# Kernel optimization log

Hardware: AMD Instinct MI355X
Metric: run time of the kernel (lower is better)

The kernel has to match this reference:

```python
import jax, jax.numpy as jnp
import numpy as np

N, T, E, E2 = 10000, 32, 320000, 160000
D, H = 128, 128
SLOPE = 0.01  # LeakyReLU negative slope (args.relu)


def _lstm_dir(x, mask, Wih, Whh, b, reverse):
    # x: [N,T,D], mask: [N,T] int; returns final hidden [N,H] honoring per-seq lengths
    xs = jnp.swapaxes(x, 0, 1)                                 # [T,N,D]
    ms = jnp.swapaxes(mask, 0, 1)[..., None].astype(x.dtype)   # [T,N,1]
    Hh = Whh.shape[1]
    h0 = jnp.zeros((x.shape[0], Hh), x.dtype)

    def step(carry, tm):
        h, c = carry
        xt, mt = tm
        g = xt @ Wih.T + h @ Whh.T + b                         # [N,4H], torch gate order i,f,g,o
        i, f, gg, o = jnp.split(g, 4, axis=-1)
        i, f, o = jax.nn.sigmoid(i), jax.nn.sigmoid(f), jax.nn.sigmoid(o)
        c_new = f * c + i * jnp.tanh(gg)
        h_new = o * jnp.tanh(c_new)
        h = mt * h_new + (1.0 - mt) * h
        c = mt * c_new + (1.0 - mt) * c
        return (h, c), None

    (h, _), _ = jax.lax.scan(step, (h0, h0), (xs, ms), reverse=reverse)
    return h


def _sage(h, src, dst, Wself, Wneigh, b):
    # DGL SAGEConv, mean aggregator: h@W_self + mean_neigh(h)@W_neigh + b
    n = h.shape[0]
    msum = jax.ops.segment_sum(h[src], dst, num_segments=n)
    deg = jax.ops.segment_sum(jnp.ones((src.shape[0],), h.dtype), dst, num_segments=n)
    neigh = msum / jnp.maximum(deg, 1.0)[:, None]
    return h @ Wself + neigh @ Wneigh + b


def setup_inputs():
    key = jax.random.key(0)
    ks = jax.random.split(key, 40)
    f = lambda i, shape: jax.random.normal(ks[i], shape, jnp.float32) * 0.05
    return dict(
        inputs_s=jax.random.randint(ks[0], (N, T), 0, 128, jnp.int32),
        inputs_sm=jnp.ones((N, T), jnp.int32),
        inputs_c=jax.random.randint(ks[1], (N,), 0, 101, jnp.int32),
        inputs_co=jax.random.randint(ks[2], (N,), 0, 92, jnp.int32),
        inputs_sl=jax.random.randint(ks[3], (N,), 0, 6, jnp.int32),
        inputs_ip=jax.random.normal(ks[4], (N, 32), jnp.float32),
        blk_src=jax.random.randint(ks[5], (E,), 0, N, jnp.int32),
        blk_dst=jax.random.randint(ks[6], (E,), 0, N, jnp.int32),
        e_src=jax.random.randint(ks[7], (E2,), 0, N, jnp.int32),
        e_dst=jax.random.randint(ks[8], (E2,), 0, N, jnp.int32),
        emb_url=f(9, (128, D)), emb_cat=f(10, (101, D)), emb_cou=f(11, (92, D)), emb_sl_t=f(12, (6, D)),
        Wih_f=f(13, (4 * D, D)), Whh_f=f(14, (4 * D, D)), b_f=f(15, (4 * D,)),
        Wih_b=f(16, (4 * D, D)), Whh_b=f(17, (4 * D, D)), b_b=f(18, (4 * D,)),
        fc_lstm_W=f(19, (2 * D, D)), fc_lstm_b=f(20, (D,)),
        attnlin_W=f(21, (H, H)), attn_W=f(22, (H, 1)), attn_b=f(23, (1,)),
        W0_self=f(24, (4, D, H)), W0_neigh=f(25, (4, D, H)), b0=f(26, (4, H)),
        Wip_self=f(27, (32, H)), Wip_neigh=f(28, (32, H)), bip=f(29, (H,)),
        W1_self=f(30, (5, H, H)), W1_neigh=f(31, (5, H, H)), b1=f(32, (5, H)),
        fc_W=f(33, (2 * H, H)), fc_b=f(34, (H,)),
        fco_W=f(35, (H, 2)), fco_b=f(36, (2,)),
    )


def reference(inputs_s, inputs_sm, inputs_c, inputs_co, inputs_sl, inputs_ip,
              blk_src, blk_dst, e_src, e_dst,
              emb_url, emb_cat, emb_cou, emb_sl_t,
              Wih_f, Whh_f, b_f, Wih_b, Whh_b, b_b,
              fc_lstm_W, fc_lstm_b, attnlin_W, attn_W, attn_b,
              W0_self, W0_neigh, b0, Wip_self, Wip_neigh, bip,
              W1_self, W1_neigh, b1, fc_W, fc_b, fco_W, fco_b):
    lrelu = lambda x: jax.nn.leaky_relu(x, SLOPE)
    # --- URL encoder: embed -> bi-LSTM -> fc (dropout is identity in eval) ---
    xu = emb_url[inputs_s]                                      # [N,T,D]
    hf = _lstm_dir(xu, inputs_sm, Wih_f, Whh_f, b_f, False)     # fwd final hidden
    hb = _lstm_dir(xu, inputs_sm, Wih_b, Whh_b, b_b, True)      # bwd final hidden
    vec_url = lrelu(jnp.concatenate([hf, hb], 1) @ fc_lstm_W + fc_lstm_b)
    # --- six-stream (here five: no rules) SAGE stacks over shared blocks ---
    h4 = jnp.stack([vec_url, emb_cat[inputs_c], emb_cou[inputs_co], emb_sl_t[inputs_sl]])  # [4,N,D]
    sage_v = jax.vmap(_sage, in_axes=(0, None, None, 0, 0, 0))
    h4 = lrelu(sage_v(h4, blk_src, blk_dst, W0_self, W0_neigh, b0))
    hip = lrelu(_sage(inputs_ip, blk_src, blk_dst, Wip_self, Wip_neigh, bip))
    hs = jnp.concatenate([h4, hip[None]], 0)                    # [5,N,H]
    hs = lrelu(sage_v(hs, blk_src, blk_dst, W1_self, W1_neigh, b1))
    hs = jnp.transpose(hs, (1, 0, 2))                           # [N,5,H]
    # --- attention fusion across streams ---
    z = jnp.einsum('nsh,ho->nso', hs, attnlin_W)                # attn_linear(h_stack)
    a = jax.nn.softmax(jnp.einsum('nso,om->nsm', z, attn_W) + attn_b, axis=1)  # [N,5,1]
    h = jnp.sum(z * a, axis=1)                                  # [N,H]
    # --- per-edge gather-concat-MLP scoring (apply_edges) ---
    cat = jnp.concatenate([h[e_src], h[e_dst]], 1)              # [E2,2H]
    score = lrelu(cat @ fc_W + fc_b) @ fco_W + fco_b            # [E2,2]
    a_src = a[e_src][..., 0]                                    # [E2,5]
    attn_e = jnp.stack([a_src, a_src], axis=1)                  # [E2,2,5]
    return score, attn_e
```

## Files before the change

### kernel.cpp

```cpp
#include <hip/hip_runtime.h>
#include <hip/hip_bf16.h>
#include <stdint.h>

typedef unsigned short u16;
typedef unsigned int   u32;
typedef __attribute__((ext_vector_type(8))) short short8;
typedef __attribute__((ext_vector_type(4))) float f32x4;
typedef __attribute__((ext_vector_type(2))) u32   u32x2;
typedef __attribute__((ext_vector_type(4))) u32   u32x4;

#define DEV static __device__ __forceinline__

constexpr int N_  = 10000;
constexpr int T_  = 32;
constexpr int E_  = 320000;
constexpr int E2_ = 160000;

DEV u16 f2bf(float f) {
    union { float f; u32 u; } v; v.f = f;
    u32 u = v.u;
    return (u16)((u + 0x7fffu + ((u >> 16) & 1u)) >> 16);
}
DEV float bf2f(u16 h) {
    union { u32 u; float f; } v; v.u = ((u32)h) << 16; return v.f;
}
DEV float asf(u32 u) {
    union { u32 u; float f; } v; v.u = u; return v.f;
}
DEV u32 cvt_pk_bf16(float lo, float hi) {
    u32 r;
    asm("v_cvt_pk_bf16_f32 %0, %1, %2" : "=v"(r) : "v"(lo), "v"(hi));
    return r;
}
DEV float lrelu(float x) { return x > 0.f ? x : 0.01f * x; }

DEV float fexp2(float x) {
#if __has_builtin(__builtin_amdgcn_exp2f)
    return __builtin_amdgcn_exp2f(x);
#else
    return exp2f(x);
#endif
}
DEV float frcp(float x) {
#if __has_builtin(__builtin_amdgcn_rcpf)
    return __builtin_amdgcn_rcpf(x);
#else
    return 1.0f / x;
#endif
}
DEV float fsig(float x)  { return frcp(1.f + fexp2(-1.4426950408889634f * x)); }
DEV float ftanh_(float x){ return 1.f - 2.f * frcp(1.f + fexp2(2.8853900817779268f * x)); }

__global__ void k_xtab(const float* __restrict__ emb,
                       const float* __restrict__ WihF, const float* __restrict__ bF,
                       const float* __restrict__ WihB, const float* __restrict__ bB,
                       u16* __restrict__ xtab) {
    int sym = blockIdx.x, dir = blockIdx.y, o = threadIdx.x;
    const float* W = dir ? WihB : WihF;
    const float* b = dir ? bB : bF;
    __shared__ float er[128];
    if (o < 128) er[o] = emb[sym * 128 + o];
    __syncthreads();
    float s = b[o];
    for (int k = 0; k < 128; k++) s += er[k] * W[o * 128 + k];
    xtab[((size_t)(dir * 128 + sym)) * 512 + o] = f2bf(s);
}

struct WtSeg { const float* W; u16* out; int Kd, Ks, Nw, tot; };
struct WtArgs { WtSeg seg[9]; };
__global__ void k_wt_all(WtArgs a) {
    WtSeg sg = a.seg[blockIdx.y];
    int i = blockIdx.x * 256 + threadIdx.x;
    if (i >= sg.tot) return;
    int k = i % sg.Kd, n = (i / sg.Kd) % sg.Nw, s = i / (sg.Kd * sg.Nw);
    float v = (k < sg.Ks) ? sg.W[((size_t)s * sg.Ks + k) * sg.Nw + n] : 0.f;
    sg.out[i] = f2bf(v);
}

__global__ __launch_bounds__(512, 2) void k_lstm(
    const u16* __restrict__ xtab,
    const int* __restrict__ syms,
    const int* __restrict__ smask,
    const float* __restrict__ WhhF,
    const float* __restrict__ WhhB,
    u16* __restrict__ hcat)
{
    __shared__ u16 h_buf0[2048];
    __shared__ u16 h_buf1[2048];
    __shared__ int sym_l[512];
    __shared__ int msk_l[512];

    int tid = threadIdx.x;
    int w = tid >> 6, l = tid & 63, l15 = l & 15, lg = l >> 4;
    int dir = blockIdx.y;
    int n0 = blockIdx.x * 16;
    const float* Whh = dir ? WhhB : WhhF;

    for (int i = tid; i < 512; i += 512) {
        int seq = i >> 5, t = i & 31;
        sym_l[t * 16 + seq] = syms[(size_t)n0 * 32 + i];
        msk_l[t * 16 + seq] = smask[(size_t)n0 * 32 + i];
    }
    for (int i = tid; i < 2048; i += 512) h_buf0[i] = 0;

    short8 aw[4][4];
#pragma unroll
    for (int gg = 0; gg < 4; gg++)
#pragma unroll
    for (int kk = 0; kk < 4; kk++) {
        const float* p = Whh + (size_t)(128 * gg + 16 * w + l15) * 128 + 32 * kk + 8 * lg;
        const float4* pp = (const float4*)p;
        float4 x0 = pp[0], x1 = pp[1];
        short8 v;
        v[0] = (short)f2bf(x0.x); v[1] = (short)f2bf(x0.y);
        v[2] = (short)f2bf(x0.z); v[3] = (short)f2bf(x0.w);
        v[4] = (short)f2bf(x1.x); v[5] = (short)f2bf(x1.y);
        v[6] = (short)f2bf(x1.z); v[7] = (short)f2bf(x1.w);
        aw[gg][kk] = v;
    }

    float hreg[4] = {0, 0, 0, 0};
    float creg[4] = {0, 0, 0, 0};
    int jb = 16 * w + 4 * lg;
    int wsk = 2 * w + (lg >> 1);
    int wof = (wsk * 16 + l15) * 8 + 4 * (lg & 1);
    const u16* xbase = xtab + (size_t)dir * 128 * 512 + jb;
    __syncthreads();

    u32x2 xt[4];
    {
        int t0 = dir ? 31 : 0;
        int sym0 = sym_l[t0 * 16 + l15];
        const u16* xr = xbase + (size_t)sym0 * 512;
#pragma unroll
        for (int gg = 0; gg < 4; gg++) xt[gg] = *(const u32x2*)(xr + gg * 128);
    }

    auto step = [&](int st, const u16* rb, u16* wb) {
        int t = dir ? (31 - st) : st;

        short8 bh[4];
#pragma unroll
        for (int kk = 0; kk < 4; kk++)
            bh[kk] = *(const short8*)&rb[((kk * 4 + lg) * 16 + l15) * 8];

        f32x4 acc[4];
#pragma unroll
        for (int gg = 0; gg < 4; gg++) {
            f32x4 a = { asf(xt[gg][0] << 16), asf(xt[gg][0] & 0xffff0000u),
                        asf(xt[gg][1] << 16), asf(xt[gg][1] & 0xffff0000u) };
#pragma unroll
            for (int kk = 0; kk < 4; kk++)
                a = __builtin_amdgcn_mfma_f32_16x16x32_bf16(aw[gg][kk], bh[kk], a, 0, 0, 0);
            acc[gg] = a;
        }

        {
            int stn = (st < 31) ? (st + 1) : 31;
            int tn = dir ? (31 - stn) : stn;
            int symn = sym_l[tn * 16 + l15];
            const u16* xr = xbase + (size_t)symn * 512;
#pragma unroll
            for (int gg = 0; gg < 4; gg++) xt[gg] = *(const u32x2*)(xr + gg * 128);
        }

        int mt_i = msk_l[t * 16 + l15];
        bool mb = mt_i != 0;
#pragma unroll
        for (int r = 0; r < 4; r++) {
            float i_ = fsig(acc[0][r]), f_ = fsig(acc[1][r]);
            float g_ = ftanh_(acc[2][r]), o_ = fsig(acc[3][r]);
            float cn = f_ * creg[r] + i_ * g_;
            float hn = o_ * ftanh_(cn);
            hreg[r] = mb ? hn : hreg[r];
            creg[r] = mb ? cn : creg[r];
        }
        u32x2 pk;
        pk[0] = cvt_pk_bf16(hreg[0], hreg[1]);
        pk[1] = cvt_pk_bf16(hreg[2], hreg[3]);
        *(u32x2*)&wb[wof] = pk;
        asm volatile("s_waitcnt lgkmcnt(0)" ::: "memory");
        __builtin_amdgcn_s_barrier();
    };

    for (int st2 = 0; st2 < 16; st2++) {
        step(2 * st2,     h_buf0, h_buf1);
        step(2 * st2 + 1, h_buf1, h_buf0);
    }

    {
        u32x2 pk;
        pk[0] = cvt_pk_bf16(hreg[0], hreg[1]);
        pk[1] = cvt_pk_bf16(hreg[2], hreg[3]);
        *(u32x2*)&hcat[(size_t)(n0 + l15) * 256 + dir * 128 + jb] = pk;
    }
}

template<int ACT, int DUAL>
__global__ __launch_bounds__(256) void k_gemm(
    const u16* __restrict__ A1, int lda1, int soA1,
    const u16* __restrict__ A2, int lda2, int soA2,
    const u16* __restrict__ B1, int soB1,
    const u16* __restrict__ B2, int soB2,
    const float* __restrict__ bias, int soBias,
    u16* __restrict__ C, int ldc, int soC, int M, int K)
{
    int s = blockIdx.y;
    A1 += (size_t)s * soA1;
    if (DUAL) A2 += (size_t)s * soA2;
    B1 += (size_t)s * soB1;
    if (DUAL) B2 += (size_t)s * soB2;
    if (bias) bias += (size_t)s * soBias;
    C += (size_t)s * soC;

    int tid = threadIdx.x;
    int w = tid >> 6, l = tid & 63, l15 = l & 15, lg = l >> 4;
    int mbase = blockIdx.x * 64 + w * 16;
    int arow = mbase + l15; if (arow >= M) arow = M - 1;

    f32x4 acc[8];
#pragma unroll
    for (int nt = 0; nt < 8; nt++) {
        float bv = bias ? bias[16 * nt + l15] : 0.f;
        acc[nt] = (f32x4){bv, bv, bv, bv};
    }
    for (int k0 = 0; k0 < K; k0 += 32) {
        int k = k0 + 8 * lg;
        short8 a1 = *(const short8*)&A1[(size_t)arow * lda1 + k];
        short8 a2;
        if (DUAL) a2 = *(const short8*)&A2[(size_t)arow * lda2 + k];
#pragma unroll
        for (int nt = 0; nt < 8; nt++) {
            short8 b1 = *(const short8*)&B1[(size_t)(16 * nt + l15) * K + k];
            acc[nt] = __builtin_amdgcn_mfma_f32_16x16x32_bf16(a1, b1, acc[nt], 0, 0, 0);
            if (DUAL) {
                short8 b2 = *(const short8*)&B2[(size_t)(16 * nt + l15) * K + k];
                acc[nt] = __builtin_amdgcn_mfma_f32_16x16x32_bf16(a2, b2, acc[nt], 0, 0, 0);
            }
        }
    }
#pragma unroll
    for (int nt = 0; nt < 8; nt++)
#pragma unroll
    for (int r = 0; r < 4; r++) {
        int m = mbase + 4 * lg + r;
        if (m < M) {
            float v = acc[nt][r];
            if (ACT == 1) v = lrelu(v);
            C[(size_t)m * ldc + 16 * nt + l15] = f2bf(v);
        }
    }
}

__global__ void k_pack(const int* __restrict__ ic, const int* __restrict__ ico,
                       const int* __restrict__ isl, const float* __restrict__ ip,
                       const float* __restrict__ ecat, const float* __restrict__ ecou,
                       const float* __restrict__ esl, u16* __restrict__ F0) {
    int n = blockIdx.x, t = threadIdx.x;
    u16* row = F0 + (size_t)n * 544;
    row[128 + t] = f2bf(ecat[(size_t)ic[n]  * 128 + t]);
    row[256 + t] = f2bf(ecou[(size_t)ico[n] * 128 + t]);
    row[384 + t] = f2bf(esl [(size_t)isl[n] * 128 + t]);
    if (t < 32) row[512 + t] = f2bf(ip[(size_t)n * 32 + t]);
}

__global__ void k_hist(const int* __restrict__ dst, int E, int* __restrict__ deg) {
    int e = blockIdx.x * 256 + threadIdx.x;
    if (e < E) atomicAdd(&deg[dst[e]], 1);
}
__global__ void k_scan(const int* __restrict__ deg, int* __restrict__ rowptr,
                       int* __restrict__ cursor, int n) {
    __shared__ int part[1024];
    int tid = threadIdx.x;
    const int CH = 10;
    int base = tid * CH;
    int s = 0;
#pragma unroll
    for (int i = 0; i < CH; i++) { int idx = base + i; if (idx < n) s += deg[idx]; }
    part[tid] = s; __syncthreads();
    for (int off = 1; off < 1024; off <<= 1) {
        int v = (tid >= off) ? part[tid - off] : 0;
        __syncthreads();
        part[tid] += v;
        __syncthreads();
    }
    int run = part[tid] - s;
    for (int i = 0; i < CH; i++) {
        int idx = base + i;
        if (idx < n) { rowptr[idx] = run; cursor[idx] = run; run += deg[idx]; }
    }
    if (tid == 1023) rowptr[n] = part[1023];
}
__global__ void k_fill(const int* __restrict__ src, const int* __restrict__ dst, int E,
                       int* __restrict__ cursor, int* __restrict__ colsrc) {
    int e = blockIdx.x * 256 + threadIdx.x;
    if (e < E) {
        int pos = atomicAdd(&cursor[dst[e]], 1);
        colsrc[pos] = src[e];
    }
}

__global__ __launch_bounds__(256) void k_agg(const u16* __restrict__ F, int C,
                                             const int* __restrict__ rowptr,
                                             const int* __restrict__ colsrc,
                                             u16* __restrict__ out, int N) {
    int w = threadIdx.x >> 6, l = threadIdx.x & 63;
    int n = blockIdx.x * 4 + w;
    if (n >= N) return;
    int chunks = C >> 3;
    int c0 = l, c1 = l + 64;
    bool has1 = c1 < chunks;
    float a0[8] = {0,0,0,0,0,0,0,0}, a1[8] = {0,0,0,0,0,0,0,0};
    int beg = rowptr[n], end = rowptr[n + 1];

    auto accum = [&](u32x4 v, float* a) {
#pragma unroll
        for (int j = 0; j < 4; j++) {
            u32 u = v[j];
            a[2*j]   += asf(u << 16);
            a[2*j+1] += asf(u & 0xffff0000u);
        }
    };

    int e = beg;
    for (; e + 8 <= end; e += 8) {
        const u32x4* rp[8];
#pragma unroll
        for (int j = 0; j < 8; j++)
            rp[j] = (const u32x4*)(F + (size_t)colsrc[e + j] * C);
        u32x4 v[8];
#pragma unroll
        for (int j = 0; j < 8; j++) v[j] = rp[j][c0];
        if (has1) {
            u32x4 u[8];
#pragma unroll
            for (int j = 0; j < 8; j++) u[j] = rp[j][c1];
#pragma unroll
            for (int j = 0; j < 8; j++) accum(v[j], a0);
#pragma unroll
            for (int j = 0; j < 8; j++) accum(u[j], a1);
        } else {
#pragma unroll
            for (int j = 0; j < 8; j++) accum(v[j], a0);
        }
    }
    for (; e + 4 <= end; e += 4) {
        const u32x4* rp[4];
#pragma unroll
        for (int j = 0; j < 4; j++)
            rp[j] = (const u32x4*)(F + (size_t)colsrc[e + j] * C);
        u32x4 v[4];
#pragma unroll
        for (int j = 0; j < 4; j++) v[j] = rp[j][c0];
        if (has1) {
            u32x4 u[4];
#pragma unroll
            for (int j = 0; j < 4; j++) u[j] = rp[j][c1];
#pragma unroll
            for (int j = 0; j < 4; j++) accum(v[j], a0);
#pragma unroll
            for (int j = 0; j < 4; j++) accum(u[j], a1);
        } else {
#pragma unroll
            for (int j = 0; j < 4; j++) accum(v[j], a0);
        }
    }
    for (; e < end; e++) {
        const u32x4* rp = (const u32x4*)(F + (size_t)colsrc[e] * C);
        accum(rp[c0], a0);
        if (has1) accum(rp[c1], a1);
    }

    int dg = end - beg; if (dg < 1) dg = 1;
    float inv = 1.f / (float)dg;
    u32x4 o0;
#pragma unroll
    for (int j = 0; j < 4; j++)
        o0[j] = (u32)f2bf(a0[2*j] * inv) | ((u32)f2bf(a0[2*j+1] * inv) << 16);
    ((u32x4*)(out + (size_t)n * C))[c0] = o0;
    if (has1) {
        u32x4 o1;
#pragma unroll
        for (int j = 0; j < 4; j++)
            o1[j] = (u32)f2bf(a1[2*j] * inv) | ((u32)f2bf(a1[2*j+1] * inv) << 16);
        ((u32x4*)(out + (size_t)n * C))[c1] = o1;
    }
}

__global__ __launch_bounds__(256) void k_attn(const u16* __restrict__ Z,
                                              const float* __restrict__ attnW,
                                              float* __restrict__ aOut,
                                              u16* __restrict__ hT, int N) {
    int w = threadIdx.x >> 6, l = threadIdx.x & 63;
    int n = blockIdx.x * 4 + w;
    if (n >= N) return;
    float wa0 = attnW[l], wa1 = attnW[l + 64];
    float z0[5], z1[5], lgt[5];
#pragma unroll
    for (int s = 0; s < 5; s++) {
        z0[s] = bf2f(Z[((size_t)(n * 5 + s)) * 128 + l]);
        z1[s] = bf2f(Z[((size_t)(n * 5 + s)) * 128 + l + 64]);
        float p = z0[s] * wa0 + z1[s] * wa1;
#pragma unroll
        for (int m = 1; m < 64; m <<= 1) p += __shfl_xor(p, m, 64);
        lgt[s] = p;
    }
    float mx = lgt[0];
#pragma unroll
    for (int s = 1; s < 5; s++) mx = fmaxf(mx, lgt[s]);
    float ex[5], sum = 0.f;
#pragma unroll
    for (int s = 0; s < 5; s++) { ex[s] = __expf(lgt[s] - mx); sum += ex[s]; }
    float a[5];
#pragma unroll
    for (int s = 0; s < 5; s++) a[s] = ex[s] / sum;
    float h0 = 0.f, h1 = 0.f;
#pragma unroll
    for (int s = 0; s < 5; s++) { h0 += a[s] * z0[s]; h1 += a[s] * z1[s]; }
    hT[(size_t)n * 128 + l] = f2bf(h0);
    hT[(size_t)n * 128 + l + 64] = f2bf(h1);
    if (l == 0) {
#pragma unroll
        for (int s = 0; s < 5; s++) aOut[(size_t)n * 5 + s] = a[s];
    }
}

__global__ __launch_bounds__(256) void k_edge(const u16* __restrict__ hT,
                                              const int* __restrict__ esrc,
                                              const int* __restrict__ edst,
                                              const u16* __restrict__ fcWt,
                                              const float* __restrict__ fcb,
                                              const float* __restrict__ fcoW,
                                              const float* __restrict__ fcob,
                                              const float* __restrict__ aA,
                                              float* __restrict__ score,
                                              float* __restrict__ attne,
                                              int E2) {
    int tid = threadIdx.x;
    int w = tid >> 6, l = tid & 63, l15 = l & 15, lg = l >> 4;
    int eb = (blockIdx.x * 4 + w) * 16;
    int arow = eb + l15; if (arow >= E2) arow = E2 - 1;
    int sn = esrc[arow], dn = edst[arow];

    f32x4 acc[8];
#pragma unroll
    for (int nt = 0; nt < 8; nt++) {
        float bv = fcb[16 * nt + l15];
        acc[nt] = (f32x4){bv, bv, bv, bv};
    }
#pragma unroll
    for (int kk = 0; kk < 8; kk++) {
        int k = 32 * kk + 8 * lg;
        const u16* ap = (k < 128) ? &hT[(size_t)sn * 128 + k]
                                  : &hT[(size_t)dn * 128 + (k - 128)];
        short8 a = *(const short8*)ap;
#pragma unroll
        for (int nt = 0; nt < 8; nt++) {
            short8 b = *(const short8*)&fcWt[(size_t)(16 * nt + l15) * 256 + k];
            acc[nt] = __builtin_amdgcn_mfma_f32_16x16x32_bf16(a, b, acc[nt], 0, 0, 0);
        }
    }
    float p0[4] = {0,0,0,0}, p1[4] = {0,0,0,0};
#pragma unroll
    for (int nt = 0; nt < 8; nt++) {
        int c = 16 * nt + l15;
        float w0 = fcoW[c * 2], w1 = fcoW[c * 2 + 1];
#pragma unroll
        for (int r = 0; r < 4; r++) {
            float hd = lrelu(acc[nt][r]);
            p0[r] += hd * w0; p1[r] += hd * w1;
        }
    }
#pragma unroll
    for (int m = 1; m < 16; m <<= 1) {
#pragma unroll
        for (int r = 0; r < 4; r++) {
            p0[r] += __shfl_xor(p0[r], m, 64);
            p1[r] += __shfl_xor(p1[r], m, 64);
        }
    }
    if (l15 == 0) {
        float b0v = fcob[0], b1v = fcob[1];
#pragma unroll
        for (int r = 0; r < 4; r++) {
            int e = eb + 4 * lg + r;
            if (e < E2) {
                score[(size_t)e * 2 + 0] = p0[r] + b0v;
                score[(size_t)e * 2 + 1] = p1[r] + b1v;
            }
        }
    }
#pragma unroll
    for (int pass = 0; pass < 3; pass++) {
        int idx = pass * 64 + l;
        if (idx < 160) {
            int e = eb + idx / 10;
            int j = idx % 10;
            int s = esrc[e];
            attne[(size_t)e * 10 + j] = aA[(size_t)s * 5 + (j >= 5 ? j - 5 : j)];
        }
    }
}

extern "C" void kernel_launch(void* const* d_in, const int* in_sizes, int n_in,
                              void* d_out, int out_size, void* d_ws, size_t ws_size,
                              hipStream_t stream) {
    const int* inp_s   = (const int*)d_in[0];
    const int* inp_sm  = (const int*)d_in[1];
    const int* inp_c   = (const int*)d_in[2];
    const int* inp_co  = (const int*)d_in[3];
    const int* inp_sl  = (const int*)d_in[4];
    const float* inp_ip = (const float*)d_in[5];
    const int* blk_src = (const int*)d_in[6];
    const int* blk_dst = (const int*)d_in[7];
    const int* e_src   = (const int*)d_in[8];
    const int* e_dst   = (const int*)d_in[9];
    const float* emb_url = (const float*)d_in[10];
    const float* emb_cat = (const float*)d_in[11];
    const float* emb_cou = (const float*)d_in[12];
    const float* emb_sl  = (const float*)d_in[13];
    const float* Wih_f = (const float*)d_in[14];
    const float* Whh_f = (const float*)d_in[15];
    const float* b_f   = (const float*)d_in[16];
    const float* Wih_b = (const float*)d_in[17];
    const float* Whh_b = (const float*)d_in[18];
    const float* b_b   = (const float*)d_in[19];
    const float* fc_lstm_W = (const float*)d_in[20];
    const float* fc_lstm_b = (const float*)d_in[21];
    const float* attnlin_W = (const float*)d_in[22];
    const float* attn_W    = (const float*)d_in[23];
    const float* W0_self  = (const float*)d_in[25];
    const float* W0_neigh = (const float*)d_in[26];
    const float* b0       = (const float*)d_in[27];
    const float* Wip_self  = (const float*)d_in[28];
    const float* Wip_neigh = (const float*)d_in[29];
    const float* bip       = (const float*)d_in[30];
    const float* W1_self  = (const float*)d_in[31];
    const float* W1_neigh = (const float*)d_in[32];
    const float* b1       = (const float*)d_in[33];
    const float* fc_W  = (const float*)d_in[34];
    const float* fc_b  = (const float*)d_in[35];
    const float* fco_W = (const float*)d_in[36];
    const float* fco_b = (const float*)d_in[37];

    char* ws = (char*)d_ws;
    size_t off = 0;
    auto alloc = [&](size_t bytes) -> char* {
        char* p = ws + off;
        off += (bytes + 255) & ~(size_t)255;
        return p;
    };
    u16* xtab      = (u16*)alloc((size_t)2 * 128 * 512 * 2);
    u16* hcat      = (u16*)alloc((size_t)N_ * 256 * 2);
    u16* wt_fclstm = (u16*)alloc((size_t)128 * 256 * 2);
    u16* wt_w05s   = (u16*)alloc((size_t)5 * 128 * 128 * 2);
    u16* wt_w05n   = (u16*)alloc((size_t)5 * 128 * 128 * 2);
    u16* wt_w1s    = (u16*)alloc((size_t)5 * 128 * 128 * 2);
    u16* wt_w1n    = (u16*)alloc((size_t)5 * 128 * 128 * 2);
    u16* wt_attn   = (u16*)alloc((size_t)128 * 128 * 2);
    u16* wt_fc     = (u16*)alloc((size_t)128 * 256 * 2);
    float* bias5   = (float*)alloc((size_t)5 * 128 * 4);
    u16* F0        = (u16*)alloc((size_t)N_ * 544 * 2);
    u16* NEI       = (u16*)alloc((size_t)N_ * 640 * 2);
    u16* F1        = (u16*)alloc((size_t)N_ * 640 * 2);
    u16* H1        = (u16*)alloc((size_t)N_ * 640 * 2);
    u16* Zb        = (u16*)alloc((size_t)N_ * 5 * 128 * 2);
    u16* hT        = (u16*)alloc((size_t)N_ * 128 * 2);
    float* aA      = (float*)alloc((size_t)N_ * 5 * 4);
    int* deg       = (int*)alloc((size_t)N_ * 4);
    int* rowptr    = (int*)alloc((size_t)(N_ + 1) * 4);
    int* cursor    = (int*)alloc((size_t)N_ * 4);
    int* colsrc    = (int*)alloc((size_t)E_ * 4);
    (void)ws_size; (void)in_sizes; (void)n_in; (void)out_size;

    float* out_score = (float*)d_out;
    float* out_attne = out_score + (size_t)2 * E2_;

    hipMemsetAsync(deg, 0, (size_t)N_ * 4, stream);
    k_hist<<<dim3((E_ + 255) / 256), dim3(256), 0, stream>>>(blk_dst, E_, deg);
    k_scan<<<dim3(1), dim3(1024), 0, stream>>>(deg, rowptr, cursor, N_);
    k_fill<<<dim3((E_ + 255) / 256), dim3(256), 0, stream>>>(blk_src, blk_dst, E_, cursor, colsrc);

    k_xtab<<<dim3(128, 2), dim3(512), 0, stream>>>(emb_url, Wih_f, b_f, Wih_b, b_b, xtab);
    {
        WtArgs a;
        a.seg[0] = {fc_lstm_W, wt_fclstm,            256, 256, 128, 1 * 128 * 256};
        a.seg[1] = {W0_self,   wt_w05s,              128, 128, 128, 4 * 128 * 128};
        a.seg[2] = {W0_neigh,  wt_w05n,              128, 128, 128, 4 * 128 * 128};
        a.seg[3] = {Wip_self,  wt_w05s + 4 * 16384,  128,  32, 128, 1 * 128 * 128};
        a.seg[4] = {Wip_neigh, wt_w05n + 4 * 16384,  128,  32, 128, 1 * 128 * 128};
        a.seg[5] = {W1_self,   wt_w1s,               128, 128, 128, 5 * 128 * 128};
        a.seg[6] = {W1_neigh,  wt_w1n,               128, 128, 128, 5 * 128 * 128};
        a.seg[7] = {attnlin_W, wt_attn,              128, 128, 128, 1 * 128 * 128};
        a.seg[8] = {fc_W,      wt_fc,                256, 256, 128, 1 * 128 * 256};
        k_wt_all<<<dim3((5 * 128 * 128 + 255) / 256, 9), dim3(256), 0, stream>>>(a);
    }
    hipMemcpyAsync(bias5, b0, 512 * sizeof(float), hipMemcpyDeviceToDevice, stream);
    hipMemcpyAsync(bias5 + 512, bip, 128 * sizeof(float), hipMemcpyDeviceToDevice, stream);

    k_lstm<<<dim3(N_ / 16, 2), dim3(512), 0, stream>>>(xtab, inp_s, inp_sm, Whh_f, Whh_b, hcat);

    k_gemm<1, 0><<<dim3((N_ + 63) / 64, 1), dim3(256), 0, stream>>>(
        hcat, 256, 0, nullptr, 0, 0, wt_fclstm, 0, nullptr, 0,
        fc_lstm_b, 0, F0, 544, 0, N_, 256);
    k_pack<<<dim3(N_), dim3(128), 0, stream>>>(inp_c, inp_co, inp_sl, inp_ip,
                                               emb_cat, emb_cou, emb_sl, F0);

    k_agg<<<dim3(N_ / 4), dim3(256), 0, stream>>>(F0, 544, rowptr, colsrc, NEI, N_);
    k_gemm<1, 1><<<dim3((N_ + 63) / 64, 5), dim3(256), 0, stream>>>(
        F0, 544, 128, NEI, 544, 128, wt_w05s, 128 * 128, wt_w05n, 128 * 128,
        bias5, 128, F1, 640, 128, N_, 128);

    k_agg<<<dim3(N_ / 4), dim3(256), 0, stream>>>(F1, 640, rowptr, colsrc, NEI, N_);
    k_gemm<1, 1><<<dim3((N_ + 63) / 64, 5), dim3(256), 0, stream>>>(
        F1, 640, 128, NEI, 640, 128, wt_w1s, 128 * 128, wt_w1n, 128 * 128,
        b1, 128, H1, 640, 128, N_, 128);

    k_gemm<0, 0><<<dim3((N_ * 5 + 63) / 64, 1), dim3(256), 0, stream>>>(
        H1, 128, 0, nullptr, 0, 0, wt_attn, 0, nullptr, 0,
        nullptr, 0, Zb, 128, 0, N_ * 5, 128);
    k_attn<<<dim3(N_ / 4), dim3(256), 0, stream>>>(Zb, attn_W, aA, hT, N_);

    k_edge<<<dim3(E2_ / 64), dim3(256), 0, stream>>>(hT, e_src, e_dst, wt_fc, fc_b,
                                                     fco_W, fco_b, aA,
                                                     out_score, out_attne, E2_);
}
```

Before: 587.4 us.

## Fuse attention GEMM with softmax, merge packing kernels, trim LSTM tail

Fuses the attention linear GEMM with the per-node softmax and weighted sum in one kernel that stages Z in shared memory, removing the Zb global round trip and one launch. Merges the fc_lstm GEMM and the embedding pack into one two-part launch, and folds the deg memset and bias copies into the weight-transpose kernel. Also skips the final LSTM step's h write and barrier and vectorizes the xtab weight loads. Each change removes launch overhead or memory traffic, at the cost of more complex kernels.

```diff
diff --git a/kernel.cpp b/kernel.cpp
--- a/kernel.cpp
+++ b/kernel.cpp
@@ -62,13 +62,28 @@
     if (o < 128) er[o] = emb[sym * 128 + o];
     __syncthreads();
     float s = b[o];
-    for (int k = 0; k < 128; k++) s += er[k] * W[o * 128 + k];
+    const float4* Wr = (const float4*)(W + (size_t)o * 128);
+    for (int k4 = 0; k4 < 32; k4++) {
+        float4 wv = Wr[k4];
+        s += er[4*k4]   * wv.x + er[4*k4+1] * wv.y
+           + er[4*k4+2] * wv.z + er[4*k4+3] * wv.w;
+    }
     xtab[((size_t)(dir * 128 + sym)) * 512 + o] = f2bf(s);
 }
 
 struct WtSeg { const float* W; u16* out; int Kd, Ks, Nw, tot; };
-struct WtArgs { WtSeg seg[9]; };
+struct WtArgs {
+    WtSeg seg[9];
+    int* deg; float* bias5; const float* b0; const float* bip;
+};
 __global__ void k_wt_all(WtArgs a) {
+    if (blockIdx.y == 9) {
+        int gid = blockIdx.x * 256 + threadIdx.x;
+        if (gid < N_) a.deg[gid] = 0;
+        int b = gid - 10240;
+        if (b >= 0 && b < 640) a.bias5[b] = (b < 512) ? a.b0[b] : a.bip[b - 512];
+        return;
+    }
     WtSeg sg = a.seg[blockIdx.y];
     int i = blockIdx.x * 256 + threadIdx.x;
     if (i >= sg.tot) return;
@@ -136,7 +151,7 @@
         for (int gg = 0; gg < 4; gg++) xt[gg] = *(const u32x2*)(xr + gg * 128);
     }
 
-    auto step = [&](int st, const u16* rb, u16* wb) {
+    auto step = [&](int st, const u16* rb, u16* wb, bool wr) {
         int t = dir ? (31 - st) : st;
 
         short8 bh[4];
@@ -155,8 +170,8 @@
             acc[gg] = a;
         }
 
-        {
-            int stn = (st < 31) ? (st + 1) : 31;
+        if (wr) {
+            int stn = st + 1;
             int tn = dir ? (31 - stn) : stn;
             int symn = sym_l[tn * 16 + l15];
             const u16* xr = xbase + (size_t)symn * 512;
@@ -175,18 +190,22 @@
             hreg[r] = mb ? hn : hreg[r];
             creg[r] = mb ? cn : creg[r];
         }
-        u32x2 pk;
-        pk[0] = cvt_pk_bf16(hreg[0], hreg[1]);
-        pk[1] = cvt_pk_bf16(hreg[2], hreg[3]);
-        *(u32x2*)&wb[wof] = pk;
-        asm volatile("s_waitcnt lgkmcnt(0)" ::: "memory");
-        __builtin_amdgcn_s_barrier();
+        if (wr) {
+            u32x2 pk;
+            pk[0] = cvt_pk_bf16(hreg[0], hreg[1]);
+            pk[1] = cvt_pk_bf16(hreg[2], hreg[3]);
+            *(u32x2*)&wb[wof] = pk;
+            asm volatile("s_waitcnt lgkmcnt(0)" ::: "memory");
+            __builtin_amdgcn_s_barrier();
+        }
     };
 
-    for (int st2 = 0; st2 < 16; st2++) {
-        step(2 * st2,     h_buf0, h_buf1);
-        step(2 * st2 + 1, h_buf1, h_buf0);
-    }
+    for (int st2 = 0; st2 < 15; st2++) {
+        step(2 * st2,     h_buf0, h_buf1, true);
+        step(2 * st2 + 1, h_buf1, h_buf0, true);
+    }
+    step(30, h_buf0, h_buf1, true);
+    step(31, h_buf1, h_buf0, false);
 
     {
         u32x2 pk;
@@ -252,16 +271,56 @@
     }
 }
 
-__global__ void k_pack(const int* __restrict__ ic, const int* __restrict__ ico,
-                       const int* __restrict__ isl, const float* __restrict__ ip,
-                       const float* __restrict__ ecat, const float* __restrict__ ecou,
-                       const float* __restrict__ esl, u16* __restrict__ F0) {
-    int n = blockIdx.x, t = threadIdx.x;
-    u16* row = F0 + (size_t)n * 544;
-    row[128 + t] = f2bf(ecat[(size_t)ic[n]  * 128 + t]);
-    row[256 + t] = f2bf(ecou[(size_t)ico[n] * 128 + t]);
-    row[384 + t] = f2bf(esl [(size_t)isl[n] * 128 + t]);
-    if (t < 32) row[512 + t] = f2bf(ip[(size_t)n * 32 + t]);
+__global__ __launch_bounds__(256) void k_fcpack(
+    const u16* __restrict__ hcat, const u16* __restrict__ Bt,
+    const float* __restrict__ bias, u16* __restrict__ F0,
+    const int* __restrict__ ic, const int* __restrict__ ico,
+    const int* __restrict__ isl, const float* __restrict__ ip,
+    const float* __restrict__ ecat, const float* __restrict__ ecou,
+    const float* __restrict__ esl, int M)
+{
+    if (blockIdx.y == 1) {
+        int gid = blockIdx.x * 256 + threadIdx.x;
+        const int TOT = N_ * 416;
+        for (int i = gid; i < TOT; i += 40192) {
+            int n = i / 416, c = i - n * 416;
+            float v;
+            if (c < 128)      v = ecat[(size_t)ic[n]  * 128 + c];
+            else if (c < 256) v = ecou[(size_t)ico[n] * 128 + (c - 128)];
+            else if (c < 384) v = esl [(size_t)isl[n] * 128 + (c - 256)];
+            else              v = ip  [(size_t)n * 32 + (c - 384)];
+            F0[(size_t)n * 544 + 128 + c] = f2bf(v);
+        }
+        return;
+    }
+    int tid = threadIdx.x;
+    int w = tid >> 6, l = tid & 63, l15 = l & 15, lg = l >> 4;
+    int mbase = blockIdx.x * 64 + w * 16;
+    int arow = mbase + l15; if (arow >= M) arow = M - 1;
+
+    f32x4 acc[8];
+#pragma unroll
+    for (int nt = 0; nt < 8; nt++) {
+        float bv = bias[16 * nt + l15];
+        acc[nt] = (f32x4){bv, bv, bv, bv};
+    }
+    for (int k0 = 0; k0 < 256; k0 += 32) {
+        int k = k0 + 8 * lg;
+        short8 a1 = *(const short8*)&hcat[(size_t)arow * 256 + k];
+#pragma unroll
+        for (int nt = 0; nt < 8; nt++) {
+            short8 b1 = *(const short8*)&Bt[(size_t)(16 * nt + l15) * 256 + k];
+            acc[nt] = __builtin_amdgcn_mfma_f32_16x16x32_bf16(a1, b1, acc[nt], 0, 0, 0);
+        }
+    }
+#pragma unroll
+    for (int nt = 0; nt < 8; nt++)
+#pragma unroll
+    for (int r = 0; r < 4; r++) {
+        int m = mbase + 4 * lg + r;
+        if (m < M)
+            F0[(size_t)m * 544 + 16 * nt + l15] = f2bf(lrelu(acc[nt][r]));
+    }
 }
 
 __global__ void k_hist(const int* __restrict__ dst, int E, int* __restrict__ deg) {
@@ -387,41 +446,84 @@
     }
 }
 
-__global__ __launch_bounds__(256) void k_attn(const u16* __restrict__ Z,
-                                              const float* __restrict__ attnW,
-                                              float* __restrict__ aOut,
-                                              u16* __restrict__ hT, int N) {
-    int w = threadIdx.x >> 6, l = threadIdx.x & 63;
-    int n = blockIdx.x * 4 + w;
-    if (n >= N) return;
-    float wa0 = attnW[l], wa1 = attnW[l + 64];
-    float z0[5], z1[5], lgt[5];
-#pragma unroll
-    for (int s = 0; s < 5; s++) {
-        z0[s] = bf2f(Z[((size_t)(n * 5 + s)) * 128 + l]);
-        z1[s] = bf2f(Z[((size_t)(n * 5 + s)) * 128 + l + 64]);
-        float p = z0[s] * wa0 + z1[s] * wa1;
-#pragma unroll
-        for (int m = 1; m < 64; m <<= 1) p += __shfl_xor(p, m, 64);
-        lgt[s] = p;
-    }
-    float mx = lgt[0];
-#pragma unroll
-    for (int s = 1; s < 5; s++) mx = fmaxf(mx, lgt[s]);
-    float ex[5], sum = 0.f;
-#pragma unroll
-    for (int s = 0; s < 5; s++) { ex[s] = __expf(lgt[s] - mx); sum += ex[s]; }
-    float a[5];
-#pragma unroll
-    for (int s = 0; s < 5; s++) a[s] = ex[s] / sum;
-    float h0 = 0.f, h1 = 0.f;
-#pragma unroll
-    for (int s = 0; s < 5; s++) { h0 += a[s] * z0[s]; h1 += a[s] * z1[s]; }
-    hT[(size_t)n * 128 + l] = f2bf(h0);
-    hT[(size_t)n * 128 + l + 64] = f2bf(h1);
-    if (l == 0) {
-#pragma unroll
-        for (int s = 0; s < 5; s++) aOut[(size_t)n * 5 + s] = a[s];
+__global__ __launch_bounds__(320) void k_zattn(
+    const u16* __restrict__ H1,
+    const u16* __restrict__ Bt,
+    const float* __restrict__ attnW,
+    float* __restrict__ aOut,
+    u16* __restrict__ hT)
+{
+    constexpr int ZP = 136;
+    __shared__ u16 zl[80 * ZP];
+    int tid = threadIdx.x;
+    int w = tid >> 6, l = tid & 63, l15 = l & 15, lg = l >> 4;
+    int rbase = blockIdx.x * 80 + w * 16;
+
+    f32x4 acc[8];
+#pragma unroll
+    for (int nt = 0; nt < 8; nt++) acc[nt] = (f32x4){0.f, 0.f, 0.f, 0.f};
+    for (int k0 = 0; k0 < 128; k0 += 32) {
+        int k = k0 + 8 * lg;
+        short8 a1 = *(const short8*)&H1[(size_t)(rbase + l15) * 128 + k];
+#pragma unroll
+        for (int nt = 0; nt < 8; nt++) {
+            short8 b1 = *(const short8*)&Bt[(size_t)(16 * nt + l15) * 128 + k];
+            acc[nt] = __builtin_amdgcn_mfma_f32_16x16x32_bf16(a1, b1, acc[nt], 0, 0, 0);
+        }
+    }
+#pragma unroll
+    for (int nt = 0; nt < 8; nt++)
+#pragma unroll
+    for (int r = 0; r < 4; r++)
+        zl[(w * 16 + 4 * lg + r) * ZP + 16 * nt + l15] = f2bf(acc[nt][r]);
+    __syncthreads();
+
+    if (tid < 256) {
+        int node = tid >> 4;
+        int j = tid & 15;
+        int d0 = j * 8;
+        float4 wa0 = *(const float4*)(attnW + d0);
+        float4 wa1 = *(const float4*)(attnW + d0 + 4);
+        float z[5][8], lgt[5];
+#pragma unroll
+        for (int s = 0; s < 5; s++) {
+            const u16* zr = &zl[(node * 5 + s) * ZP + d0];
+            u32x4 v = *(const u32x4*)zr;
+#pragma unroll
+            for (int q = 0; q < 4; q++) {
+                z[s][2*q]   = asf(v[q] << 16);
+                z[s][2*q+1] = asf(v[q] & 0xffff0000u);
+            }
+            float p = z[s][0]*wa0.x + z[s][1]*wa0.y + z[s][2]*wa0.z + z[s][3]*wa0.w
+                    + z[s][4]*wa1.x + z[s][5]*wa1.y + z[s][6]*wa1.z + z[s][7]*wa1.w;
+#pragma unroll
+            for (int m = 1; m < 16; m <<= 1) p += __shfl_xor(p, m, 64);
+            lgt[s] = p;
+        }
+        float mx = lgt[0];
+#pragma unroll
+        for (int s = 1; s < 5; s++) mx = fmaxf(mx, lgt[s]);
+        float ex[5], sum = 0.f;
+#pragma unroll
+        for (int s = 0; s < 5; s++) { ex[s] = __expf(lgt[s] - mx); sum += ex[s]; }
+        float inv = 1.f / sum;
+        float a[5];
+#pragma unroll
+        for (int s = 0; s < 5; s++) a[s] = ex[s] * inv;
+        float h[8] = {0,0,0,0,0,0,0,0};
+#pragma unroll
+        for (int s = 0; s < 5; s++)
+#pragma unroll
+            for (int q = 0; q < 8; q++) h[q] += a[s] * z[s][q];
+        int gn = blockIdx.x * 16 + node;
+        u32x4 o;
+#pragma unroll
+        for (int q = 0; q < 4; q++) o[q] = cvt_pk_bf16(h[2*q], h[2*q+1]);
+        *(u32x4*)&hT[(size_t)gn * 128 + d0] = o;
+        if (j == 0) {
+#pragma unroll
+            for (int s = 0; s < 5; s++) aOut[(size_t)gn * 5 + s] = a[s];
+        }
     }
 }
 
@@ -564,7 +666,6 @@
     u16* NEI       = (u16*)alloc((size_t)N_ * 640 * 2);
     u16* F1        = (u16*)alloc((size_t)N_ * 640 * 2);
     u16* H1        = (u16*)alloc((size_t)N_ * 640 * 2);
-    u16* Zb        = (u16*)alloc((size_t)N_ * 5 * 128 * 2);
     u16* hT        = (u16*)alloc((size_t)N_ * 128 * 2);
     float* aA      = (float*)alloc((size_t)N_ * 5 * 4);
     int* deg       = (int*)alloc((size_t)N_ * 4);
@@ -575,11 +676,6 @@
 
     float* out_score = (float*)d_out;
     float* out_attne = out_score + (size_t)2 * E2_;
-
-    hipMemsetAsync(deg, 0, (size_t)N_ * 4, stream);
-    k_hist<<<dim3((E_ + 255) / 256), dim3(256), 0, stream>>>(blk_dst, E_, deg);
-    k_scan<<<dim3(1), dim3(1024), 0, stream>>>(deg, rowptr, cursor, N_);
-    k_fill<<<dim3((E_ + 255) / 256), dim3(256), 0, stream>>>(blk_src, blk_dst, E_, cursor, colsrc);
 
     k_xtab<<<dim3(128, 2), dim3(512), 0, stream>>>(emb_url, Wih_f, b_f, Wih_b, b_b, xtab);
     {
@@ -593,18 +689,19 @@
         a.seg[6] = {W1_neigh,  wt_w1n,               128, 128, 128, 5 * 128 * 128};
         a.seg[7] = {attnlin_W, wt_attn,              128, 128, 128, 1 * 128 * 128};
         a.seg[8] = {fc_W,      wt_fc,                256, 256, 128, 1 * 128 * 256};
-        k_wt_all<<<dim3((5 * 128 * 128 + 255) / 256, 9), dim3(256), 0, stream>>>(a);
-    }
-    hipMemcpyAsync(bias5, b0, 512 * sizeof(float), hipMemcpyDeviceToDevice, stream);
-    hipMemcpyAsync(bias5 + 512, bip, 128 * sizeof(float), hipMemcpyDeviceToDevice, stream);
+        a.deg = deg; a.bias5 = bias5; a.b0 = b0; a.bip = bip;
+        k_wt_all<<<dim3((5 * 128 * 128 + 255) / 256, 10), dim3(256), 0, stream>>>(a);
+    }
+
+    k_hist<<<dim3((E_ + 255) / 256), dim3(256), 0, stream>>>(blk_dst, E_, deg);
+    k_scan<<<dim3(1), dim3(1024), 0, stream>>>(deg, rowptr, cursor, N_);
+    k_fill<<<dim3((E_ + 255) / 256), dim3(256), 0, stream>>>(blk_src, blk_dst, E_, cursor, colsrc);
 
     k_lstm<<<dim3(N_ / 16, 2), dim3(512), 0, stream>>>(xtab, inp_s, inp_sm, Whh_f, Whh_b, hcat);
 
-    k_gemm<1, 0><<<dim3((N_ + 63) / 64, 1), dim3(256), 0, stream>>>(
-        hcat, 256, 0, nullptr, 0, 0, wt_fclstm, 0, nullptr, 0,
-        fc_lstm_b, 0, F0, 544, 0, N_, 256);
-    k_pack<<<dim3(N_), dim3(128), 0, stream>>>(inp_c, inp_co, inp_sl, inp_ip,
-                                               emb_cat, emb_cou, emb_sl, F0);
+    k_fcpack<<<dim3((N_ + 63) / 64, 2), dim3(256), 0, stream>>>(
+        hcat, wt_fclstm, fc_lstm_b, F0,
+        inp_c, inp_co, inp_sl, inp_ip, emb_cat, emb_cou, emb_sl, N_);
 
     k_agg<<<dim3(N_ / 4), dim3(256), 0, stream>>>(F0, 544, rowptr, colsrc, NEI, N_);
     k_gemm<1, 1><<<dim3((N_ + 63) / 64, 5), dim3(256), 0, stream>>>(
@@ -616,10 +713,7 @@
         F1, 640, 128, NEI, 640, 128, wt_w1s, 128 * 128, wt_w1n, 128 * 128,
         b1, 128, H1, 640, 128, N_, 128);
 
-    k_gemm<0, 0><<<dim3((N_ * 5 + 63) / 64, 1), dim3(256), 0, stream>>>(
-        H1, 128, 0, nullptr, 0, 0, wt_attn, 0, nullptr, 0,
-        nullptr, 0, Zb, 128, 0, N_ * 5, 128);
-    k_attn<<<dim3(N_ / 4), dim3(256), 0, stream>>>(Zb, attn_W, aA, hT, N_);
+    k_zattn<<<dim3(N_ / 16), dim3(320), 0, stream>>>(H1, wt_attn, attn_W, aA, hT);
 
     k_edge<<<dim3(E2_ / 64), dim3(256), 0, stream>>>(hT, e_src, e_dst, wt_fc, fc_b,
                                                      fco_W, fco_b, aA,
```

Result: no change. 596.1 us (+1.5%).
